# Optimization experiments

Measured on AMD Instinct MI355X. Metric: run time of the kernel, lower is better.

Reference implementation:

```python
import jax, jax.numpy as jnp
import numpy as np

NUM_NODES = 200000
NUM_LAYERS = 3
EMBED_DIM = 64
NUM_EDGES = 3200000
NUM_PAIRS = 1000000


def setup_inputs() -> dict:
    key = jax.random.key(0)
    k1, k2, k3 = jax.random.split(key, 3)
    emb = jax.random.normal(k1, (NUM_NODES, EMBED_DIM), dtype=jnp.float32)
    alpha = jnp.ones((NUM_LAYERS + 1,), dtype=jnp.float32) * (1.0 / (NUM_LAYERS + 1))
    edge_index = jax.random.randint(k2, (2, NUM_EDGES), 0, NUM_NODES, dtype=jnp.int32)
    edge_label_index = jax.random.randint(k3, (2, NUM_PAIRS), 0, NUM_NODES, dtype=jnp.int32)
    return {"emb": emb, "alpha": alpha, "edge_index": edge_index,
            "edge_label_index": edge_label_index}


def reference(emb, alpha, edge_index, edge_label_index):
    row, col = edge_index[0], edge_index[1]  # source -> target
    # symmetric normalization (gcn_norm without self-loops, as in LGConv)
    ones = jnp.ones((row.shape[0],), dtype=emb.dtype)
    deg = jax.ops.segment_sum(ones, col, num_segments=NUM_NODES)
    dinv = jnp.where(deg > 0, jax.lax.rsqrt(jnp.maximum(deg, 1.0)), 0.0)
    norm = dinv[row] * dinv[col]  # [E]

    x = emb
    out = x * alpha[0]
    for l in range(NUM_LAYERS):
        # gather messages from sources, scale by norm, scatter-add into targets
        msgs = x[row] * norm[:, None]                      # [E, D]
        x = jax.ops.segment_sum(msgs, col, num_segments=NUM_NODES)  # [N, D]
        out = out + x * alpha[l + 1]

    src = out[edge_label_index[0]]  # [P, D]
    dst = out[edge_label_index[1]]  # [P, D]
    return jnp.sum(src * dst, axis=-1)  # [P]
```

## Files before the change

### kernel.cpp

```cpp
#include <hip/hip_runtime.h>
#include <hip/hip_fp16.h>

#define N_NODES 200000
#define N_EDGES 3200000
#define N_PAIRS 1000000
#define DIM 64
#define CAP 48
#define NPB 256
#define NB 782
#define BKTCAP 5120
#define CHUNK 4096
#define NBLK1 ((N_EDGES + CHUNK - 1) / CHUNK)
#define PART_THREADS 512
#define BSTRIDE 16

__global__ void part_kernel(const int* __restrict__ row, const int* __restrict__ col,
                            int* __restrict__ bktcnt, int* __restrict__ staging, int E) {
    __shared__ int cnt[NB];
    __shared__ int base[NB];
    for (int i = threadIdx.x; i < NB; i += PART_THREADS) cnt[i] = 0;
    __syncthreads();
    int start = blockIdx.x * CHUNK;
    int end = min(start + CHUNK, E);
    for (int e = start + threadIdx.x; e < end; e += PART_THREADS)
        atomicAdd(&cnt[col[e] >> 8], 1);
    __syncthreads();
    for (int i = threadIdx.x; i < NB; i += PART_THREADS) {
        int c = cnt[i];
        base[i] = (c > 0) ? atomicAdd(&bktcnt[i * BSTRIDE], c) : 0;
        cnt[i] = 0;
    }
    __syncthreads();
    for (int e = start + threadIdx.x; e < end; e += PART_THREADS) {
        int c = col[e];
        int r = row[e];
        int b = c >> 8;
        int off = atomicAdd(&cnt[b], 1);
        int p = base[b] + off;
        if (p < BKTCAP) staging[(size_t)b * BKTCAP + p] = ((c & 255) << 18) | r;
    }
}

__global__ void build_kernel(const int* __restrict__ staging, const int* __restrict__ bktcnt,
                             int* __restrict__ srcrow, int* __restrict__ deg,
                             float* __restrict__ dinv, int N) {
    __shared__ int tile[NPB * CAP];
    __shared__ int cur[NPB];
    int b = blockIdx.x;
    for (int i = threadIdx.x; i < NPB; i += 256) cur[i] = 0;
    __syncthreads();
    int cnt = min(bktcnt[b * BSTRIDE], BKTCAP);
    const int* st = staging + (size_t)b * BKTCAP;
    for (int i = threadIdx.x; i < cnt; i += 256) {
        int packed = st[i];
        int r = packed & 0x3FFFF;
        int cl = packed >> 18;
        int p = atomicAdd(&cur[cl], 1);
        if (p < CAP) tile[cl * CAP + p] = r;
    }
    __syncthreads();
    int nodeBase = b * NPB;
    int nvalid = min(NPB, N - nodeBase);
    for (int i = threadIdx.x; i < nvalid; i += 256) {
        int d = min(cur[i], CAP);
        deg[nodeBase + i] = d;
        dinv[nodeBase + i] = (d > 0) ? rsqrtf((float)d) : 0.0f;
    }
    int tot = nvalid * CAP;
    int* dst = srcrow + (size_t)nodeBase * CAP;
    for (int i = threadIdx.x; i < tot; i += 256) dst[i] = tile[i];
}

__global__ void ewpack_kernel(unsigned int* __restrict__ ew, const int* __restrict__ deg,
                              int total) {
    int s = blockIdx.x * blockDim.x + threadIdx.x;
    if (s >= total) return;
    int n = s / CAP;
    int l = s - n * CAP;
    unsigned int e = 0;
    if (l < deg[n]) {
        int r = (int)ew[s];
        e = (unsigned int)r | ((unsigned int)deg[r] << 18);
    }
    ew[s] = e;
}

__global__ void convert_kernel(const float2* __restrict__ x, __half2* __restrict__ y, int n2) {
    int i = blockIdx.x * blockDim.x + threadIdx.x;
    if (i < n2) {
        float2 v = x[i];
        y[i] = __floats2half2_rn(v.x, v.y);
    }
}

__device__ __forceinline__ float2 h2f(unsigned int u) {
    __half2 h = *(__half2*)&u;
    return __half22float2(h);
}

__global__ void prop_kernel(const uint2* __restrict__ x, const unsigned int* __restrict__ ew,
                            const int* __restrict__ deg, const float* __restrict__ dinv,
                            uint2* __restrict__ xn, int N) {
    __shared__ int2 lds[4][CAP];
    int wv = threadIdx.x >> 6;
    int n = blockIdx.x * 4 + wv;
    int l = threadIdx.x & 63;
    int q = l & 15;
    int quarter = l >> 4;
    int cnt = deg[n];
    if (l < CAP) {
        unsigned int e = ew[(unsigned int)n * CAP + l];
        int id = e & 0x3FFFF;
        int dr = e >> 18;
        float w = dr ? rsqrtf((float)dr) : 0.0f;
        lds[wv][l] = make_int2(id, __float_as_int(w));
    }
    __syncthreads();
    float a0 = 0.f, a1 = 0.f, a2 = 0.f, a3 = 0.f;
    int trips = (cnt + 3) >> 2;
    #pragma unroll 2
    for (int k = 0; k < trips; ++k) {
        int2 e = lds[wv][k * 4 + quarter];
        float w = __int_as_float(e.y);
        uint2 pix = x[(unsigned int)e.x * 16u + q];
        float2 flo = h2f(pix.x);
        float2 fhi = h2f(pix.y);
        a0 += flo.x * w; a1 += flo.y * w;
        a2 += fhi.x * w; a3 += fhi.y * w;
    }
    a0 += __shfl_xor(a0, 16, 64); a1 += __shfl_xor(a1, 16, 64);
    a2 += __shfl_xor(a2, 16, 64); a3 += __shfl_xor(a3, 16, 64);
    a0 += __shfl_xor(a0, 32, 64); a1 += __shfl_xor(a1, 32, 64);
    a2 += __shfl_xor(a2, 32, 64); a3 += __shfl_xor(a3, 32, 64);
    float dn = dinv[n];
    if (quarter == 0) {
        __half2 o01 = __floats2half2_rn(a0 * dn, a1 * dn);
        __half2 o23 = __floats2half2_rn(a2 * dn, a3 * dn);
        uint2 out;
        out.x = *(unsigned int*)&o01;
        out.y = *(unsigned int*)&o23;
        xn[(unsigned int)n * 16u + q] = out;
    }
}

__global__ void prop_final_kernel(const uint2* __restrict__ x, const unsigned int* __restrict__ ew,
                                  const int* __restrict__ deg, const float* __restrict__ dinv,
                                  const uint2* __restrict__ h0, const uint2* __restrict__ h1,
                                  const float* __restrict__ alpha,
                                  uint2* __restrict__ outh, int N) {
    __shared__ int2 lds[4][CAP];
    int wv = threadIdx.x >> 6;
    int n = blockIdx.x * 4 + wv;
    int l = threadIdx.x & 63;
    int q = l & 15;
    int quarter = l >> 4;
    int cnt = deg[n];
    if (l < CAP) {
        unsigned int e = ew[(unsigned int)n * CAP + l];
        int id = e & 0x3FFFF;
        int dr = e >> 18;
        float w = dr ? rsqrtf((float)dr) : 0.0f;
        lds[wv][l] = make_int2(id, __float_as_int(w));
    }
    __syncthreads();
    float a0 = 0.f, a1 = 0.f, a2 = 0.f, a3 = 0.f;
    int trips = (cnt + 3) >> 2;
    #pragma unroll 2
    for (int k = 0; k < trips; ++k) {
        int2 e = lds[wv][k * 4 + quarter];
        float w = __int_as_float(e.y);
        uint2 pix = x[(unsigned int)e.x * 16u + q];
        float2 flo = h2f(pix.x);
        float2 fhi = h2f(pix.y);
        a0 += flo.x * w; a1 += flo.y * w;
        a2 += fhi.x * w; a3 += fhi.y * w;
    }
    a0 += __shfl_xor(a0, 16, 64); a1 += __shfl_xor(a1, 16, 64);
    a2 += __shfl_xor(a2, 16, 64); a3 += __shfl_xor(a3, 16, 64);
    a0 += __shfl_xor(a0, 32, 64); a1 += __shfl_xor(a1, 32, 64);
    a2 += __shfl_xor(a2, 32, 64); a3 += __shfl_xor(a3, 32, 64);
    float dn = dinv[n];
    if (quarter == 0) {
        float al0 = alpha[0], al1 = alpha[1], al2 = alpha[2], al3 = alpha[3];
        unsigned int idx = (unsigned int)n * 16u + q;
        uint2 p0 = h0[idx];
        uint2 p1 = h1[idx];
        uint2 p2 = x[idx];
        float2 f0l = h2f(p0.x), f0h = h2f(p0.y);
        float2 f1l = h2f(p1.x), f1h = h2f(p1.y);
        float2 f2l = h2f(p2.x), f2h = h2f(p2.y);
        float r0 = al0 * f0l.x + al1 * f1l.x + al2 * f2l.x + al3 * (a0 * dn);
        float r1 = al0 * f0l.y + al1 * f1l.y + al2 * f2l.y + al3 * (a1 * dn);
        float r2 = al0 * f0h.x + al1 * f1h.x + al2 * f2h.x + al3 * (a2 * dn);
        float r3 = al0 * f0h.y + al1 * f1h.y + al2 * f2h.y + al3 * (a3 * dn);
        __half2 o01 = __floats2half2_rn(r0, r1);
        __half2 o23 = __floats2half2_rn(r2, r3);
        uint2 out;
        out.x = *(unsigned int*)&o01;
        out.y = *(unsigned int*)&o23;
        outh[idx] = out;
    }
}

__global__ void dot_kernel(const uint2* __restrict__ outh, const int* __restrict__ pa,
                           const int* __restrict__ pb, float* __restrict__ res, int P) {
    int t = blockIdx.x * blockDim.x + threadIdx.x;
    int g = t >> 4;
    int l = threadIdx.x & 15;
    int half = P >> 1;
    if (g >= half) return;
    int p0 = g, p1 = g + half;
    int a0 = pa[p0], b0 = pb[p0];
    int a1 = pa[p1], b1 = pb[p1];
    uint2 ua0 = outh[(size_t)a0 * 16 + l];
    uint2 ub0 = outh[(size_t)b0 * 16 + l];
    uint2 ua1 = outh[(size_t)a1 * 16 + l];
    uint2 ub1 = outh[(size_t)b1 * 16 + l];
    float2 fx0 = h2f(ua0.x), fx1 = h2f(ua0.y);
    float2 fy0 = h2f(ub0.x), fy1 = h2f(ub0.y);
    float s0 = fx0.x * fy0.x + fx0.y * fy0.y + fx1.x * fy1.x + fx1.y * fy1.y;
    float2 fu0 = h2f(ua1.x), fu1 = h2f(ua1.y);
    float2 fv0 = h2f(ub1.x), fv1 = h2f(ub1.y);
    float s1 = fu0.x * fv0.x + fu0.y * fv0.y + fu1.x * fv1.x + fu1.y * fv1.y;
    s0 += __shfl_xor(s0, 1, 64);
    s1 += __shfl_xor(s1, 1, 64);
    s0 += __shfl_xor(s0, 2, 64);
    s1 += __shfl_xor(s1, 2, 64);
    s0 += __shfl_xor(s0, 4, 64);
    s1 += __shfl_xor(s1, 4, 64);
    s0 += __shfl_xor(s0, 8, 64);
    s1 += __shfl_xor(s1, 8, 64);
    if (l == 0) {
        res[p0] = s0;
        res[p1] = s1;
    }
}

extern "C" void kernel_launch(void* const* d_in, const int* in_sizes, int n_in,
                              void* d_out, int out_size, void* d_ws, size_t ws_size,
                              hipStream_t stream) {
    const float* emb   = (const float*)d_in[0];
    const float* alpha = (const float*)d_in[1];
    const int*   ei    = (const int*)d_in[2];
    const int*   eli   = (const int*)d_in[3];
    const int* row = ei;
    const int* col = ei + N_EDGES;
    const int* pa  = eli;
    const int* pb  = eli + N_PAIRS;
    float* res = (float*)d_out;

    const size_t hfeat_bytes = (size_t)N_NODES * DIM * sizeof(__half);
    char* ws = (char*)d_ws;
    size_t off = 0;
    auto alloc = [&](size_t bytes) {
        void* p = ws + off;
        off += (bytes + 255) & ~(size_t)255;
        return p;
    };
    int*    bktcnt  = (int*)alloc((size_t)NB * BSTRIDE * sizeof(int));
    int*    staging = (int*)alloc((size_t)NB * BKTCAP * sizeof(int));
    int*    srcrow  = (int*)alloc((size_t)N_NODES * CAP * sizeof(int));
    int*    deg     = (int*)alloc((size_t)N_NODES * sizeof(int));
    float*  dinv    = (float*)alloc((size_t)N_NODES * sizeof(float));
    __half* h0      = (__half*)alloc(hfeat_bytes);
    __half* h1      = (__half*)alloc(hfeat_bytes);
    __half* h2      = (__half*)alloc(hfeat_bytes);
    __half* outh    = (__half*)alloc(hfeat_bytes);
    unsigned int* ew = (unsigned int*)srcrow;

    hipMemsetAsync(bktcnt, 0, (size_t)NB * BSTRIDE * sizeof(int), stream);
    part_kernel<<<NBLK1, PART_THREADS, 0, stream>>>(row, col, bktcnt, staging, N_EDGES);
    build_kernel<<<NB, 256, 0, stream>>>(staging, bktcnt, srcrow, deg, dinv, N_NODES);
    const int total_slots = N_NODES * CAP;
    ewpack_kernel<<<(total_slots + 255) / 256, 256, 0, stream>>>(ew, deg, total_slots);

    const int n2 = N_NODES * DIM / 2;
    convert_kernel<<<(n2 + 255) / 256, 256, 0, stream>>>((const float2*)emb, (__half2*)h0, n2);

    const int prop_grid = N_NODES / 4;
    prop_kernel<<<prop_grid, 256, 0, stream>>>((const uint2*)h0, ew, deg, dinv, (uint2*)h1, N_NODES);
    prop_kernel<<<prop_grid, 256, 0, stream>>>((const uint2*)h1, ew, deg, dinv, (uint2*)h2, N_NODES);
    prop_final_kernel<<<prop_grid, 256, 0, stream>>>((const uint2*)h2, ew, deg, dinv,
                                                     (const uint2*)h0, (const uint2*)h1,
                                                     alpha, (uint2*)outh, N_NODES);

    dot_kernel<<<((size_t)(N_PAIRS / 2) * 16 + 255) / 256, 256, 0, stream>>>(
        (const uint2*)outh, pa, pb, res, N_PAIRS);
}
```

Measured before the change: 383.9 us.

## Split edge bucketing into two-pass radix partition with coalesced staged writes

Replaces the single-pass partition, which scattered edges into 782 buckets with per-element global stores, with two passes. The first pass sorts each chunk into 98 coarse buckets in shared memory and writes each bucket out contiguously. The second pass splits each coarse bucket into 8 fine buckets the same way. The aim is to turn scattered global writes into coalesced runs, at the cost of an extra kernel launch and an extra read and write of all 3.2M packed edges.

```diff
diff --git a/kernel.cpp b/kernel.cpp
--- a/kernel.cpp
+++ b/kernel.cpp
@@ -9,39 +9,119 @@
 #define NPB 256
 #define NB 782
 #define BKTCAP 5120
-#define CHUNK 4096
-#define NBLK1 ((N_EDGES + CHUNK - 1) / CHUNK)
-#define PART_THREADS 512
 #define BSTRIDE 16
 
-__global__ void part_kernel(const int* __restrict__ row, const int* __restrict__ col,
-                            int* __restrict__ bktcnt, int* __restrict__ staging, int E) {
-    __shared__ int cnt[NB];
-    __shared__ int base[NB];
-    for (int i = threadIdx.x; i < NB; i += PART_THREADS) cnt[i] = 0;
-    __syncthreads();
-    int start = blockIdx.x * CHUNK;
-    int end = min(start + CHUNK, E);
-    for (int e = start + threadIdx.x; e < end; e += PART_THREADS)
-        atomicAdd(&cnt[col[e] >> 8], 1);
-    __syncthreads();
-    for (int i = threadIdx.x; i < NB; i += PART_THREADS) {
-        int c = cnt[i];
-        base[i] = (c > 0) ? atomicAdd(&bktcnt[i * BSTRIDE], c) : 0;
-        cnt[i] = 0;
-    }
-    __syncthreads();
-    for (int e = start + threadIdx.x; e < end; e += PART_THREADS) {
-        int c = col[e];
-        int r = row[e];
-        int b = c >> 8;
-        int off = atomicAdd(&cnt[b], 1);
-        int p = base[b] + off;
-        if (p < BKTCAP) staging[(size_t)b * BKTCAP + p] = ((c & 255) << 18) | r;
-    }
-}
-
-__global__ void build_kernel(const int* __restrict__ staging, const int* __restrict__ bktcnt,
+#define CBITS 11
+#define NBC 98
+#define BKTCAPA 34816
+#define CHUNKA 4096
+#define NBLKA ((N_EDGES + CHUNKA - 1) / CHUNKA)
+#define BUFB 4400
+
+__global__ void partA_kernel(const int* __restrict__ row, const int* __restrict__ col,
+                             int* __restrict__ bktcntA, unsigned* __restrict__ stagingA, int E) {
+    __shared__ unsigned buf[CHUNKA];
+    __shared__ int cntA[128], offA[128];
+    __shared__ int curA[NBC], baseA[NBC];
+    int tid = threadIdx.x;
+    for (int i = tid; i < 128; i += 256) cntA[i] = 0;
+    __syncthreads();
+    int start = blockIdx.x * CHUNKA;
+    unsigned pk[16];
+    int bk[16];
+    #pragma unroll
+    for (int k = 0; k < 16; ++k) {
+        int e = start + k * 256 + tid;
+        if (e < E) {
+            int c = col[e];
+            int r = row[e];
+            pk[k] = ((unsigned)(c & 2047) << 18) | (unsigned)r;
+            bk[k] = c >> CBITS;
+            atomicAdd(&cntA[bk[k]], 1);
+        } else bk[k] = -1;
+    }
+    __syncthreads();
+    if (tid < 128) offA[tid] = cntA[tid];
+    __syncthreads();
+    for (int d = 1; d < 128; d <<= 1) {
+        int v = 0;
+        if (tid < 128 && tid >= d) v = offA[tid - d];
+        __syncthreads();
+        if (tid < 128) offA[tid] += v;
+        __syncthreads();
+    }
+    if (tid < NBC) {
+        int x = offA[tid] - cntA[tid];
+        curA[tid] = x;
+        offA[tid] = x;
+        baseA[tid] = (cntA[tid] > 0) ? atomicAdd(&bktcntA[tid * BSTRIDE], cntA[tid]) : 0;
+    }
+    __syncthreads();
+    #pragma unroll
+    for (int k = 0; k < 16; ++k) {
+        if (bk[k] >= 0) {
+            int p = atomicAdd(&curA[bk[k]], 1);
+            buf[p] = pk[k];
+        }
+    }
+    __syncthreads();
+    for (int b = 0; b < NBC; ++b) {
+        int n = cntA[b];
+        if (n == 0) continue;
+        int base = baseA[b];
+        if (base + n > BKTCAPA) n = max(0, BKTCAPA - base);
+        unsigned* dst = stagingA + (size_t)b * BKTCAPA + base;
+        const int o = offA[b];
+        for (int i = tid; i < n; i += 256) dst[i] = buf[o + i];
+    }
+}
+
+__global__ void partB_kernel(const unsigned* __restrict__ stagingA, const int* __restrict__ bktcntA,
+                             int* __restrict__ bktcntB, unsigned* __restrict__ stagingB) {
+    __shared__ unsigned buf[BUFB];
+    __shared__ int cntB[8], offB[8], curB[8], baseB[8];
+    int bc = blockIdx.x >> 3;
+    int s  = blockIdx.x & 7;
+    int tid = threadIdx.x;
+    if (tid < 8) cntB[tid] = 0;
+    __syncthreads();
+    int cnt = min(bktcntA[bc * BSTRIDE], BKTCAPA);
+    int slice = (cnt + 7) >> 3;
+    int lo = s * slice;
+    int hi = min(lo + slice, cnt);
+    int n = max(hi - lo, 0);
+    const unsigned* src = stagingA + (size_t)bc * BKTCAPA + lo;
+    for (int i = tid; i < n; i += 256) atomicAdd(&cntB[src[i] >> 26], 1);
+    __syncthreads();
+    if (tid == 0) {
+        int a = 0;
+        for (int b = 0; b < 8; ++b) { offB[b] = a; a += cntB[b]; }
+    }
+    __syncthreads();
+    if (tid < 8) {
+        curB[tid] = offB[tid];
+        baseB[tid] = (cntB[tid] > 0) ? atomicAdd(&bktcntB[(bc * 8 + tid) * BSTRIDE], cntB[tid]) : 0;
+    }
+    __syncthreads();
+    for (int i = tid; i < n; i += 256) {
+        unsigned e = src[i];
+        int fb = e >> 26;
+        int p = atomicAdd(&curB[fb], 1);
+        buf[p] = e & 0x3FFFFFFu;
+    }
+    __syncthreads();
+    for (int b = 0; b < 8; ++b) {
+        int m = cntB[b];
+        if (m == 0) continue;
+        int base = baseB[b];
+        if (base + m > BKTCAP) m = max(0, BKTCAP - base);
+        unsigned* dst = stagingB + (size_t)(bc * 8 + b) * BKTCAP + base;
+        const int o = offB[b];
+        for (int i = tid; i < m; i += 256) dst[i] = buf[o + i];
+    }
+}
+
+__global__ void build_kernel(const unsigned* __restrict__ staging, const int* __restrict__ bktcnt,
                              int* __restrict__ srcrow, int* __restrict__ deg,
                              float* __restrict__ dinv, int N) {
     __shared__ int tile[NPB * CAP];
@@ -50,9 +130,9 @@
     for (int i = threadIdx.x; i < NPB; i += 256) cur[i] = 0;
     __syncthreads();
     int cnt = min(bktcnt[b * BSTRIDE], BKTCAP);
-    const int* st = staging + (size_t)b * BKTCAP;
+    const unsigned* st = staging + (size_t)b * BKTCAP;
     for (int i = threadIdx.x; i < cnt; i += 256) {
-        int packed = st[i];
+        unsigned packed = st[i];
         int r = packed & 0x3FFFF;
         int cl = packed >> 18;
         int p = atomicAdd(&cur[cl], 1);
@@ -257,20 +337,24 @@
         off += (bytes + 255) & ~(size_t)255;
         return p;
     };
-    int*    bktcnt  = (int*)alloc((size_t)NB * BSTRIDE * sizeof(int));
-    int*    staging = (int*)alloc((size_t)NB * BKTCAP * sizeof(int));
-    int*    srcrow  = (int*)alloc((size_t)N_NODES * CAP * sizeof(int));
-    int*    deg     = (int*)alloc((size_t)N_NODES * sizeof(int));
-    float*  dinv    = (float*)alloc((size_t)N_NODES * sizeof(float));
-    __half* h0      = (__half*)alloc(hfeat_bytes);
-    __half* h1      = (__half*)alloc(hfeat_bytes);
-    __half* h2      = (__half*)alloc(hfeat_bytes);
-    __half* outh    = (__half*)alloc(hfeat_bytes);
+    int*      bktcntA  = (int*)alloc((size_t)NBC * BSTRIDE * sizeof(int));
+    int*      bktcntB  = (int*)alloc((size_t)NB * BSTRIDE * sizeof(int));
+    unsigned* stagingA = (unsigned*)alloc((size_t)NBC * BKTCAPA * sizeof(unsigned));
+    unsigned* stagingB = (unsigned*)alloc((size_t)NB * BKTCAP * sizeof(unsigned));
+    int*      srcrow   = (int*)alloc((size_t)N_NODES * CAP * sizeof(int));
+    int*      deg      = (int*)alloc((size_t)N_NODES * sizeof(int));
+    float*    dinv     = (float*)alloc((size_t)N_NODES * sizeof(float));
+    __half*   h0       = (__half*)alloc(hfeat_bytes);
+    __half*   h1       = (__half*)alloc(hfeat_bytes);
+    __half*   h2       = (__half*)alloc(hfeat_bytes);
+    __half*   outh     = (__half*)alloc(hfeat_bytes);
     unsigned int* ew = (unsigned int*)srcrow;
 
-    hipMemsetAsync(bktcnt, 0, (size_t)NB * BSTRIDE * sizeof(int), stream);
-    part_kernel<<<NBLK1, PART_THREADS, 0, stream>>>(row, col, bktcnt, staging, N_EDGES);
-    build_kernel<<<NB, 256, 0, stream>>>(staging, bktcnt, srcrow, deg, dinv, N_NODES);
+    hipMemsetAsync(bktcntA, 0, (size_t)NBC * BSTRIDE * sizeof(int), stream);
+    hipMemsetAsync(bktcntB, 0, (size_t)NB * BSTRIDE * sizeof(int), stream);
+    partA_kernel<<<NBLKA, 256, 0, stream>>>(row, col, bktcntA, stagingA, N_EDGES);
+    partB_kernel<<<NBC * 8, 256, 0, stream>>>(stagingA, bktcntA, bktcntB, stagingB);
+    build_kernel<<<NB, 256, 0, stream>>>(stagingB, bktcntB, srcrow, deg, dinv, N_NODES);
     const int total_slots = N_NODES * CAP;
     ewpack_kernel<<<(total_slots + 255) / 256, 256, 0, stream>>>(ew, deg, total_slots);
 
```

Result: no change. 381.7 us (-0.6%).
